# Kernel tuning notes

Hardware: AMD Instinct MI355X
Metric: run time of the kernel (lower is better)

Reference implementation:

```python
import jax, jax.numpy as jnp
import numpy as np

B, C, H, W = 64, 512, 8, 8
K = 100            # num_class
H1, HID, L = 64, 128, 32   # ae_hidden[0], fixed hidd, ae_latent
CLIP = 100.0       # CSSRClassifier.clip_len
RED = -0.1         # model='pcssr' -> -1, times gamma=0.1
PUSH_THRESH = 10000.0


def setup_inputs() -> dict:
    key = jax.random.key(0)
    ks = jax.random.split(key, 9)
    s = lambda fan_in: 1.0 / np.sqrt(fan_in)  # kaiming-ish 1x1 conv init scale
    return {
        "x": jax.random.normal(ks[0], (B, C, H, W), jnp.float32),
        "ycls": jax.random.randint(ks[1], (B,), 0, K),
        "safe_margin_all": jax.random.normal(ks[2], (K,), jnp.float32),
        "safe_distance_all": jax.random.normal(ks[3], (K,), jnp.float32),
        "W1": jax.random.normal(ks[4], (K, H1, C), jnp.float32) * s(C),
        "W2": jax.random.normal(ks[5], (K, HID, H1), jnp.float32) * s(H1),
        "W3": jax.random.normal(ks[6], (K, L, HID), jnp.float32) * s(HID),
        "prototypes": jax.random.normal(ks[7], (K, L, H, W), jnp.float32),
        "prototypes1": jax.random.normal(ks[8], (K, L, H, W), jnp.float32),
    }


def reference(x, ycls, safe_margin_all, safe_distance_all, W1, W2, W3, prototypes, prototypes1):
    P = H * W
    xf = x.reshape(B, C, P)
    # per-class 1x1-conv encoder (tanh after every conv), batched over classes k
    h = jnp.tanh(jnp.einsum('koc,bcp->kbop', W1, xf))      # [K,B,H1,P]
    h = jnp.tanh(jnp.einsum('koi,kbip->kbop', W2, h))      # [K,B,HID,P]
    lt = jnp.tanh(jnp.einsum('koi,kbip->kbop', W3, h))     # [K,B,L,P]
    p = prototypes.reshape(K, 1, L, P)
    p1 = prototypes1.reshape(K, 1, L, P)
    # squared-L2 distance over channel dim, scaled by reduction, clipped
    er = jnp.clip(jnp.sum((lt - p) ** 2, axis=2) * RED, -CLIP, CLIP)    # [K,B,P]
    er1 = jnp.clip(jnp.sum((lt - p1) ** 2, axis=2) * RED, -CLIP, CLIP)  # [K,B,P]
    # training losses (pull on er1, push on er), vectorized across classes
    f = jnp.sum(er, axis=2)    # [K,B] spatial-summed errors
    f1 = jnp.sum(er1, axis=2)  # [K,B]
    cls_ids = jnp.arange(K)[:, None]
    mask_eq = (ycls[None, :] == cls_ids).astype(f.dtype)   # [K,B]
    n_eq = jnp.sum(mask_eq, axis=1)
    pull = jnp.sum(jnp.where(n_eq > 0,
                             jnp.sum(f1 * mask_eq, axis=1) / jnp.maximum(n_eq, 1.0),
                             0.0))
    comb = (1.0 - mask_eq) * (f < PUSH_THRESH).astype(f.dtype)
    n_comb = jnp.sum(comb, axis=1)
    push = jnp.sum(jnp.where(n_comb > 0,
                             jnp.sum(f * comb, axis=1) / jnp.maximum(n_comb, 1.0),
                             0.0))
    # cat per-class [B,1,H,W] errors along dim 1 -> [B,K,H,W]
    logits = jnp.transpose(er, (1, 0, 2)).reshape(B, K, H, W)
    logits1 = jnp.transpose(er1, (1, 0, 2)).reshape(B, K, H, W)
    return logits, logits1, pull, push
```

## Files before the change

### kernel.cpp

```cpp
#include <hip/hip_runtime.h>

typedef short  s16x8  __attribute__((ext_vector_type(8)));
typedef float  f32x16 __attribute__((ext_vector_type(16)));
typedef unsigned short u16;
typedef unsigned long long u64b;

#define MFMA32(a,b,c) __builtin_amdgcn_mfma_f32_32x32x16_bf16((a),(b),(c),0,0,0)
#define KCLS 100

__device__ __forceinline__ u16 f2bf(float f) {
  return (u16)(__builtin_bit_cast(unsigned, f) >> 16);
}

__device__ __forceinline__ float tanh_fast(float x) {
  float e = __builtin_amdgcn_exp2f(x * 2.8853900817779268f);
  return 1.0f - 2.0f * __builtin_amdgcn_rcpf(e + 1.0f);
}

__device__ __forceinline__ void ld_lds16(const void* g, void* l) {
  __builtin_amdgcn_global_load_lds(
      (const __attribute__((address_space(1))) unsigned char*)g,
      (__attribute__((address_space(3))) unsigned char*)l, 16, 0, 0);
}

__global__ void prep(const float* __restrict__ x, const float* __restrict__ w1,
                     const float* __restrict__ w2, const float* __restrict__ w3,
                     u16* __restrict__ xF, u16* __restrict__ W1F,
                     u16* __restrict__ W2F, u16* __restrict__ W3F,
                     float* __restrict__ out2) {
  __shared__ float tile[64][65];
  const int bid = blockIdx.x, t = threadIdx.x;
  if (bid == 0 && t < 2) out2[t] = 0.f;
  if (bid < 512) {
    const int b = bid >> 3, ck = bid & 7;
    #pragma unroll
    for (int j = 0; j < 4; j++) {
      int e4 = j * 1024 + t * 4;
      int c = e4 >> 6, p0 = e4 & 63;
      float4 v = *(const float4*)(x + ((size_t)b * 512 + ck * 64 + c) * 64 + p0);
      tile[c][p0] = v.x; tile[c][p0 + 1] = v.y; tile[c][p0 + 2] = v.z; tile[c][p0 + 3] = v.w;
    }
    __syncthreads();
    #pragma unroll
    for (int i = 0; i < 2; i++) {
      int s = i * 256 + t;
      int ksl = s >> 7, ph = (s >> 6) & 1, lane = s & 63;
      int cb = ksl * 16 + (lane >> 5) * 8, pp = ph * 32 + (lane & 31);
      u16 o[8];
      #pragma unroll
      for (int jj = 0; jj < 8; jj++) o[jj] = f2bf(tile[cb + jj][pp]);
      *(uint4*)(xF + (((size_t)b * 64 + (ck * 4 + ksl) * 2 + ph) * 512) + lane * 8) = *(uint4*)o;
    }
  } else if (bid < 1312) {
    int base = (bid - 512) * 512;
    #pragma unroll
    for (int i = 0; i < 2; i++) {
      int s = base + i * 256 + t;
      int frag = s >> 6, lane = s & 63;
      int k = frag >> 6, fr = frag & 63;
      int m = (fr & 1) * 32 + (lane & 31);
      int c0 = (fr >> 1) * 16 + (lane >> 5) * 8;
      const float* src = w1 + ((size_t)k * 64 + m) * 512 + c0;
      float4 a = *(const float4*)src, b4 = *(const float4*)(src + 4);
      u16 o[8] = { f2bf(a.x), f2bf(a.y), f2bf(a.z), f2bf(a.w),
                   f2bf(b4.x), f2bf(b4.y), f2bf(b4.z), f2bf(b4.w) };
      *(uint4*)(W1F + ((size_t)frag * 512) + lane * 8) = *(uint4*)o;
    }
  } else if (bid < 1512) {
    int base = (bid - 1312) * 512;
    #pragma unroll
    for (int i = 0; i < 2; i++) {
      int s = base + i * 256 + t;
      int frag = s >> 6, lane = s & 63;
      int k = frag >> 4, fr = frag & 15;
      int m = (fr & 3) * 32 + (lane & 31);
      int c0 = (fr >> 2) * 16 + (lane >> 5) * 8;
      const float* src = w2 + ((size_t)k * 128 + m) * 64 + c0;
      float4 a = *(const float4*)src, b4 = *(const float4*)(src + 4);
      u16 o[8] = { f2bf(a.x), f2bf(a.y), f2bf(a.z), f2bf(a.w),
                   f2bf(b4.x), f2bf(b4.y), f2bf(b4.z), f2bf(b4.w) };
      *(uint4*)(W2F + ((size_t)frag * 512) + lane * 8) = *(uint4*)o;
    }
  } else {
    int base = (bid - 1512) * 512;
    #pragma unroll
    for (int i = 0; i < 2; i++) {
      int s = base + i * 256 + t;
      int frag = s >> 6, lane = s & 63;
      int k = frag >> 3, kb = frag & 7;
      int m = lane & 31;
      int c0 = kb * 16 + (lane >> 5) * 8;
      const float* src = w3 + ((size_t)k * 32 + m) * 128 + c0;
      float4 a = *(const float4*)src, b4 = *(const float4*)(src + 4);
      u16 o[8] = { f2bf(a.x), f2bf(a.y), f2bf(a.z), f2bf(a.w),
                   f2bf(b4.x), f2bf(b4.y), f2bf(b4.z), f2bf(b4.w) };
      *(uint4*)(W3F + ((size_t)frag * 512) + lane * 8) = *(uint4*)o;
    }
  }
}

__global__ __launch_bounds__(256, 4) void cssr_main(
    const u16* __restrict__ W1F, const u16* __restrict__ W2F, const u16* __restrict__ W3F,
    const u16* __restrict__ xF, const float* __restrict__ protos,
    const float* __restrict__ protos1, float* __restrict__ out,
    float* __restrict__ fw, float* __restrict__ f1w)
{
  __shared__ u16 pool[16384];
  __shared__ float red[8];
  u16 (*sB)[2][4][512] = (u16(*)[2][4][512])pool;
  u16 (*h1f)[4][512]   = (u16(*)[4][512])(pool + 8192);
  u16 (*h2f)[4][512]   = (u16(*)[4][512])pool;

  const int bid = blockIdx.x;
  const int k = bid >> 5, b0 = (bid & 31) * 2;
  const int tid = threadIdx.x, w = tid >> 6, lane = tid & 63;
  const int nhalf = lane >> 5, nn = lane & 31;
  const int mt = w >> 1, ntp = w & 1;

  #pragma unroll
  for (int i = 0; i < 2; i++) {
    int f = 2 * w + i, ksl = f >> 2, nt = f & 3;
    const u16* gp = xF + (((size_t)(b0 + (nt >> 1)) * 64 + ksl * 2 + (nt & 1)) * 512) + lane * 8;
    ld_lds16(gp, &sB[0][ksl][nt][0]);
  }
  __syncthreads();

  f32x16 acc1[2] = {};
  for (int ch = 0; ch < 16; ch++) {
    const int pb = ch & 1;
    if (ch < 15) {
      #pragma unroll
      for (int i = 0; i < 2; i++) {
        int f = 2 * w + i, ksl = f >> 2, nt = f & 3;
        int g = (ch + 1) * 2 + ksl;
        const u16* gp = xF + (((size_t)(b0 + (nt >> 1)) * 64 + g * 2 + (nt & 1)) * 512) + lane * 8;
        ld_lds16(gp, &sB[pb ^ 1][ksl][nt][0]);
      }
    }
    #pragma unroll
    for (int ksl = 0; ksl < 2; ksl++) {
      int g = ch * 2 + ksl;
      s16x8 A = *(const s16x8*)(W1F + (((size_t)k * 64 + g * 2 + mt) * 512) + lane * 8);
      #pragma unroll
      for (int ntl = 0; ntl < 2; ntl++) {
        s16x8 B = *(const s16x8*)&sB[pb][ksl][ntp * 2 + ntl][lane * 8];
        acc1[ntl] = MFMA32(A, B, acc1[ntl]);
      }
    }
    __syncthreads();
  }

  #pragma unroll
  for (int ntl = 0; ntl < 2; ntl++) {
    int nt = ntp * 2 + ntl;
    #pragma unroll
    for (int g = 0; g < 4; g++) {
      u16 hv[4];
      #pragma unroll
      for (int q = 0; q < 4; q++) hv[q] = f2bf(tanh_fast(acc1[ntl][g * 4 + q]));
      int kbg = mt * 2 + (g >> 1);
      int tl  = (g & 1) * 32 + nn;
      *(u64b*)&h1f[kbg][nt][tl * 8 + nhalf * 4] = *(u64b*)hv;
    }
  }
  __syncthreads();

  f32x16 acc2[2][2] = {};
  #pragma unroll
  for (int kb = 0; kb < 4; kb++) {
    s16x8 A0 = *(const s16x8*)(W2F + (((size_t)k * 16 + kb * 4 + (mt * 2 + 0)) * 512) + lane * 8);
    s16x8 A1 = *(const s16x8*)(W2F + (((size_t)k * 16 + kb * 4 + (mt * 2 + 1)) * 512) + lane * 8);
    #pragma unroll
    for (int ntl = 0; ntl < 2; ntl++) {
      s16x8 B = *(const s16x8*)&h1f[kb][ntp * 2 + ntl][lane * 8];
      acc2[0][ntl] = MFMA32(A0, B, acc2[0][ntl]);
      acc2[1][ntl] = MFMA32(A1, B, acc2[1][ntl]);
    }
  }
  __syncthreads();

  #pragma unroll
  for (int i = 0; i < 2; i++) {
    #pragma unroll
    for (int ntl = 0; ntl < 2; ntl++) {
      int nt = ntp * 2 + ntl;
      #pragma unroll
      for (int g = 0; g < 4; g++) {
        u16 hv[4];
        #pragma unroll
        for (int q = 0; q < 4; q++) hv[q] = f2bf(tanh_fast(acc2[i][ntl][g * 4 + q]));
        int kbg2 = (mt * 2 + i) * 2 + (g >> 1);
        int tl   = (g & 1) * 32 + nn;
        *(u64b*)&h2f[kbg2][nt][tl * 8 + nhalf * 4] = *(u64b*)hv;
      }
    }
  }
  __syncthreads();

  f32x16 acc3 = {};
  #pragma unroll
  for (int kb = 0; kb < 8; kb++) {
    s16x8 A = *(const s16x8*)(W3F + (((size_t)k * 8 + kb) * 512) + lane * 8);
    s16x8 B = *(const s16x8*)&h2f[kb][w][lane * 8];
    acc3 = MFMA32(A, B, acc3);
  }

  const int b = b0 + (w >> 1);
  const int p = (w & 1) * 32 + nn;
  const float* pr  = protos  + (size_t)k * 2048;
  const float* pr1 = protos1 + (size_t)k * 2048;
  float d2 = 0.f, d21 = 0.f;
  #pragma unroll
  for (int g = 0; g < 4; g++) {
    #pragma unroll
    for (int q = 0; q < 4; q++) {
      int m = q + 8 * g + 4 * nhalf;
      float lt = tanh_fast(acc3[g * 4 + q]);
      float d = lt - pr [m * 64 + p];  d2  += d * d;
      float e = lt - pr1[m * 64 + p];  d21 += e * e;
    }
  }
  d2 += __shfl_xor(d2, 32); d21 += __shfl_xor(d21, 32);
  float er  = fminf(fmaxf(d2  * -0.1f, -100.f), 100.f);
  float er1 = fminf(fmaxf(d21 * -0.1f, -100.f), 100.f);
  if (nhalf == 0) {
    out[(size_t)b * 6400 + k * 64 + p]          = er;
    out[409600 + (size_t)b * 6400 + k * 64 + p] = er1;
  }
  float s = er, s1 = er1;
  s += __shfl_xor(s, 1);  s1 += __shfl_xor(s1, 1);
  s += __shfl_xor(s, 2);  s1 += __shfl_xor(s1, 2);
  s += __shfl_xor(s, 4);  s1 += __shfl_xor(s1, 4);
  s += __shfl_xor(s, 8);  s1 += __shfl_xor(s1, 8);
  s += __shfl_xor(s, 16); s1 += __shfl_xor(s1, 16);
  if (lane == 0) { red[w] = s; red[4 + w] = s1; }
  __syncthreads();
  if (tid < 2)      fw [k * 64 + b0 + tid]       = red[tid * 2] + red[tid * 2 + 1];
  else if (tid < 4) f1w[k * 64 + b0 + (tid - 2)] = red[4 + (tid - 2) * 2] + red[5 + (tid - 2) * 2];
}

__global__ void finalize(const float* __restrict__ f, const float* __restrict__ f1,
                         const int* __restrict__ ycls, float* __restrict__ out2) {
  const int k = blockIdx.x, b = threadIdx.x;
  float fv = f[k * 64 + b], f1v = f1[k * 64 + b];
  bool eq = (ycls[b] == k);
  bool cb = (!eq) && (fv < 10000.f);
  float s1 = eq ? f1v : 0.f, ne = eq ? 1.f : 0.f;
  float s  = cb ? fv  : 0.f, nc = cb ? 1.f : 0.f;
  #pragma unroll
  for (int o = 1; o < 64; o <<= 1) {
    s1 += __shfl_xor(s1, o); ne += __shfl_xor(ne, o);
    s  += __shfl_xor(s,  o); nc += __shfl_xor(nc, o);
  }
  if (b == 0) {
    if (ne > 0.f) atomicAdd(&out2[0], s1 / ne);
    if (nc > 0.f) atomicAdd(&out2[1], s / nc);
  }
}

extern "C" void kernel_launch(void* const* d_in, const int* in_sizes, int n_in,
                              void* d_out, int out_size, void* d_ws, size_t ws_size,
                              hipStream_t stream) {
  const float* x     = (const float*)d_in[0];
  const int*   ycls  = (const int*)d_in[1];
  const float* W1    = (const float*)d_in[4];
  const float* W2    = (const float*)d_in[5];
  const float* W3    = (const float*)d_in[6];
  const float* prot  = (const float*)d_in[7];
  const float* prot1 = (const float*)d_in[8];
  float* out = (float*)d_out;

  char* ws = (char*)d_ws;
  u16*  xFb = (u16*)(ws);
  u16*  W1F = (u16*)(ws + 4194304);
  u16*  W2F = (u16*)(ws + 10747904);
  u16*  W3F = (u16*)(ws + 12386304);
  float* fw  = (float*)(ws + 13205504);
  float* f1w = (float*)(ws + 13231104);

  prep<<<1612, 256, 0, stream>>>(x, W1, W2, W3, xFb, W1F, W2F, W3F, out + 819200);
  cssr_main<<<KCLS * 32, 256, 0, stream>>>(W1F, W2F, W3F, xFb, prot, prot1, out, fw, f1w);
  finalize<<<KCLS, 64, 0, stream>>>(fw, f1w, ycls, out + 819200);
}
```

Baseline: 151.0 us.

## Make each wave own a full sample-half chain and fuse finalize via last-block reduction

Restructures the main kernel so each wave computes all three encoder layers for its own (batch, spatial-half) column. Layer 1 now reads x fragments straight from global memory instead of through a double-buffered shared-memory pipeline, and intermediates stay in a private per-wave LDS slice, so block-wide barriers between layers go away. The separate finalize launch is replaced by atomic accumulation of per-class sums plus a last-block-done counter, whose final block computes pull and push. The cost is that each wave recomputes full W1/W2 work per column, which raises weight-fragment global loads, and the per-class sums now depend on atomics and a grid-wide completion counter.

```diff
diff --git a/kernel.cpp b/kernel.cpp
--- a/kernel.cpp
+++ b/kernel.cpp
@@ -17,20 +17,18 @@
   return 1.0f - 2.0f * __builtin_amdgcn_rcpf(e + 1.0f);
 }
 
-__device__ __forceinline__ void ld_lds16(const void* g, void* l) {
-  __builtin_amdgcn_global_load_lds(
-      (const __attribute__((address_space(1))) unsigned char*)g,
-      (__attribute__((address_space(3))) unsigned char*)l, 16, 0, 0);
-}
-
 __global__ void prep(const float* __restrict__ x, const float* __restrict__ w1,
                      const float* __restrict__ w2, const float* __restrict__ w3,
                      u16* __restrict__ xF, u16* __restrict__ W1F,
                      u16* __restrict__ W2F, u16* __restrict__ W3F,
+                     float* __restrict__ fz, unsigned* __restrict__ done,
                      float* __restrict__ out2) {
   __shared__ float tile[64][65];
   const int bid = blockIdx.x, t = threadIdx.x;
-  if (bid == 0 && t < 2) out2[t] = 0.f;
+  if (bid == 0) {
+    if (t < 2) out2[t] = 0.f;
+    if (t == 2) *done = 0u;
+  }
   if (bid < 512) {
     const int b = bid >> 3, ck = bid & 7;
     #pragma unroll
@@ -81,7 +79,7 @@
                    f2bf(b4.x), f2bf(b4.y), f2bf(b4.z), f2bf(b4.w) };
       *(uint4*)(W2F + ((size_t)frag * 512) + lane * 8) = *(uint4*)o;
     }
-  } else {
+  } else if (bid < 1612) {
     int base = (bid - 1512) * 512;
     #pragma unroll
     for (int i = 0; i < 2; i++) {
@@ -96,117 +94,91 @@
                    f2bf(b4.x), f2bf(b4.y), f2bf(b4.z), f2bf(b4.w) };
       *(uint4*)(W3F + ((size_t)frag * 512) + lane * 8) = *(uint4*)o;
     }
+  } else {
+    int i4 = (bid - 1612) * 256 + t;
+    if (i4 < 3200) {
+      float4 z = {0.f, 0.f, 0.f, 0.f};
+      *(float4*)(fz + (size_t)i4 * 4) = z;
+    }
   }
 }
 
 __global__ __launch_bounds__(256, 4) void cssr_main(
     const u16* __restrict__ W1F, const u16* __restrict__ W2F, const u16* __restrict__ W3F,
     const u16* __restrict__ xF, const float* __restrict__ protos,
-    const float* __restrict__ protos1, float* __restrict__ out,
-    float* __restrict__ fw, float* __restrict__ f1w)
+    const float* __restrict__ protos1, const int* __restrict__ ycls,
+    float* __restrict__ out, float* __restrict__ fw, float* __restrict__ f1w,
+    unsigned* __restrict__ done, float* __restrict__ out2)
 {
   __shared__ u16 pool[16384];
-  __shared__ float red[8];
-  u16 (*sB)[2][4][512] = (u16(*)[2][4][512])pool;
-  u16 (*h1f)[4][512]   = (u16(*)[4][512])(pool + 8192);
-  u16 (*h2f)[4][512]   = (u16(*)[4][512])pool;
+  __shared__ int isLast;
 
   const int bid = blockIdx.x;
   const int k = bid >> 5, b0 = (bid & 31) * 2;
   const int tid = threadIdx.x, w = tid >> 6, lane = tid & 63;
   const int nhalf = lane >> 5, nn = lane & 31;
-  const int mt = w >> 1, ntp = w & 1;
-
-  #pragma unroll
-  for (int i = 0; i < 2; i++) {
-    int f = 2 * w + i, ksl = f >> 2, nt = f & 3;
-    const u16* gp = xF + (((size_t)(b0 + (nt >> 1)) * 64 + ksl * 2 + (nt & 1)) * 512) + lane * 8;
-    ld_lds16(gp, &sB[0][ksl][nt][0]);
-  }
-  __syncthreads();
+  const int b = b0 + (w >> 1), ph = w & 1;
+
+  u16* wls = pool + (w << 12);
 
   f32x16 acc1[2] = {};
-  for (int ch = 0; ch < 16; ch++) {
-    const int pb = ch & 1;
-    if (ch < 15) {
-      #pragma unroll
-      for (int i = 0; i < 2; i++) {
-        int f = 2 * w + i, ksl = f >> 2, nt = f & 3;
-        int g = (ch + 1) * 2 + ksl;
-        const u16* gp = xF + (((size_t)(b0 + (nt >> 1)) * 64 + g * 2 + (nt & 1)) * 512) + lane * 8;
-        ld_lds16(gp, &sB[pb ^ 1][ksl][nt][0]);
-      }
-    }
-    #pragma unroll
-    for (int ksl = 0; ksl < 2; ksl++) {
-      int g = ch * 2 + ksl;
-      s16x8 A = *(const s16x8*)(W1F + (((size_t)k * 64 + g * 2 + mt) * 512) + lane * 8);
-      #pragma unroll
-      for (int ntl = 0; ntl < 2; ntl++) {
-        s16x8 B = *(const s16x8*)&sB[pb][ksl][ntp * 2 + ntl][lane * 8];
-        acc1[ntl] = MFMA32(A, B, acc1[ntl]);
-      }
-    }
-    __syncthreads();
-  }
-
-  #pragma unroll
-  for (int ntl = 0; ntl < 2; ntl++) {
-    int nt = ntp * 2 + ntl;
+  const u16* xb = xF + (((size_t)b * 64 + ph) * 512) + lane * 8;
+  const u16* wA = W1F + ((size_t)k * 64 * 512) + lane * 8;
+  #pragma unroll 4
+  for (int g = 0; g < 32; g++) {
+    s16x8 B  = *(const s16x8*)(xb + g * 1024);
+    s16x8 A0 = *(const s16x8*)(wA + g * 1024);
+    s16x8 A1 = *(const s16x8*)(wA + g * 1024 + 512);
+    acc1[0] = MFMA32(A0, B, acc1[0]);
+    acc1[1] = MFMA32(A1, B, acc1[1]);
+  }
+
+  #pragma unroll
+  for (int mt = 0; mt < 2; mt++) {
     #pragma unroll
     for (int g = 0; g < 4; g++) {
       u16 hv[4];
       #pragma unroll
-      for (int q = 0; q < 4; q++) hv[q] = f2bf(tanh_fast(acc1[ntl][g * 4 + q]));
-      int kbg = mt * 2 + (g >> 1);
+      for (int q = 0; q < 4; q++) hv[q] = f2bf(tanh_fast(acc1[mt][g * 4 + q]));
+      int kb = mt * 2 + (g >> 1);
+      int tl = (g & 1) * 32 + nn;
+      *(u64b*)&wls[kb * 512 + tl * 8 + nhalf * 4] = *(u64b*)hv;
+    }
+  }
+
+  f32x16 acc2[4] = {};
+  #pragma unroll
+  for (int kb = 0; kb < 4; kb++) {
+    s16x8 B = *(const s16x8*)&wls[kb * 512 + lane * 8];
+    #pragma unroll
+    for (int m4 = 0; m4 < 4; m4++) {
+      s16x8 A = *(const s16x8*)(W2F + (((size_t)k * 16) + kb * 4 + m4) * 512 + lane * 8);
+      acc2[m4] = MFMA32(A, B, acc2[m4]);
+    }
+  }
+
+  #pragma unroll
+  for (int m4 = 0; m4 < 4; m4++) {
+    #pragma unroll
+    for (int g = 0; g < 4; g++) {
+      u16 hv[4];
+      #pragma unroll
+      for (int q = 0; q < 4; q++) hv[q] = f2bf(tanh_fast(acc2[m4][g * 4 + q]));
+      int kb2 = m4 * 2 + (g >> 1);
       int tl  = (g & 1) * 32 + nn;
-      *(u64b*)&h1f[kbg][nt][tl * 8 + nhalf * 4] = *(u64b*)hv;
-    }
-  }
-  __syncthreads();
-
-  f32x16 acc2[2][2] = {};
-  #pragma unroll
-  for (int kb = 0; kb < 4; kb++) {
-    s16x8 A0 = *(const s16x8*)(W2F + (((size_t)k * 16 + kb * 4 + (mt * 2 + 0)) * 512) + lane * 8);
-    s16x8 A1 = *(const s16x8*)(W2F + (((size_t)k * 16 + kb * 4 + (mt * 2 + 1)) * 512) + lane * 8);
-    #pragma unroll
-    for (int ntl = 0; ntl < 2; ntl++) {
-      s16x8 B = *(const s16x8*)&h1f[kb][ntp * 2 + ntl][lane * 8];
-      acc2[0][ntl] = MFMA32(A0, B, acc2[0][ntl]);
-      acc2[1][ntl] = MFMA32(A1, B, acc2[1][ntl]);
-    }
-  }
-  __syncthreads();
-
-  #pragma unroll
-  for (int i = 0; i < 2; i++) {
-    #pragma unroll
-    for (int ntl = 0; ntl < 2; ntl++) {
-      int nt = ntp * 2 + ntl;
-      #pragma unroll
-      for (int g = 0; g < 4; g++) {
-        u16 hv[4];
-        #pragma unroll
-        for (int q = 0; q < 4; q++) hv[q] = f2bf(tanh_fast(acc2[i][ntl][g * 4 + q]));
-        int kbg2 = (mt * 2 + i) * 2 + (g >> 1);
-        int tl   = (g & 1) * 32 + nn;
-        *(u64b*)&h2f[kbg2][nt][tl * 8 + nhalf * 4] = *(u64b*)hv;
-      }
-    }
-  }
-  __syncthreads();
+      *(u64b*)&wls[kb2 * 512 + tl * 8 + nhalf * 4] = *(u64b*)hv;
+    }
+  }
 
   f32x16 acc3 = {};
   #pragma unroll
   for (int kb = 0; kb < 8; kb++) {
-    s16x8 A = *(const s16x8*)(W3F + (((size_t)k * 8 + kb) * 512) + lane * 8);
-    s16x8 B = *(const s16x8*)&h2f[kb][w][lane * 8];
+    s16x8 A = *(const s16x8*)(W3F + (((size_t)k * 8) + kb) * 512 + lane * 8);
+    s16x8 B = *(const s16x8*)&wls[kb * 512 + lane * 8];
     acc3 = MFMA32(A, B, acc3);
   }
 
-  const int b = b0 + (w >> 1);
-  const int p = (w & 1) * 32 + nn;
+  const int p = ph * 32 + nn;
   const float* pr  = protos  + (size_t)k * 2048;
   const float* pr1 = protos1 + (size_t)k * 2048;
   float d2 = 0.f, d21 = 0.f;
@@ -233,28 +205,39 @@
   s += __shfl_xor(s, 4);  s1 += __shfl_xor(s1, 4);
   s += __shfl_xor(s, 8);  s1 += __shfl_xor(s1, 8);
   s += __shfl_xor(s, 16); s1 += __shfl_xor(s1, 16);
-  if (lane == 0) { red[w] = s; red[4 + w] = s1; }
+  if (lane == 0) {
+    atomicAdd(&fw [k * 64 + b], s);
+    atomicAdd(&f1w[k * 64 + b], s1);
+  }
+
+  __threadfence();
+  if (tid == 0) isLast = (atomicAdd(done, 1u) == (unsigned)(KCLS * 32 - 1));
   __syncthreads();
-  if (tid < 2)      fw [k * 64 + b0 + tid]       = red[tid * 2] + red[tid * 2 + 1];
-  else if (tid < 4) f1w[k * 64 + b0 + (tid - 2)] = red[4 + (tid - 2) * 2] + red[5 + (tid - 2) * 2];
-}
-
-__global__ void finalize(const float* __restrict__ f, const float* __restrict__ f1,
-                         const int* __restrict__ ycls, float* __restrict__ out2) {
-  const int k = blockIdx.x, b = threadIdx.x;
-  float fv = f[k * 64 + b], f1v = f1[k * 64 + b];
-  bool eq = (ycls[b] == k);
-  bool cb = (!eq) && (fv < 10000.f);
-  float s1 = eq ? f1v : 0.f, ne = eq ? 1.f : 0.f;
-  float s  = cb ? fv  : 0.f, nc = cb ? 1.f : 0.f;
-  #pragma unroll
-  for (int o = 1; o < 64; o <<= 1) {
-    s1 += __shfl_xor(s1, o); ne += __shfl_xor(ne, o);
-    s  += __shfl_xor(s,  o); nc += __shfl_xor(nc, o);
-  }
-  if (b == 0) {
-    if (ne > 0.f) atomicAdd(&out2[0], s1 / ne);
-    if (nc > 0.f) atomicAdd(&out2[1], s / nc);
+  if (isLast) {
+    __threadfence();
+    int yv = ycls[lane];
+    float pull = 0.f, push = 0.f;
+    for (int k2 = w; k2 < KCLS; k2 += 4) {
+      float fv  = __hip_atomic_load(&fw [k2 * 64 + lane], __ATOMIC_RELAXED, __HIP_MEMORY_SCOPE_AGENT);
+      float f1v = __hip_atomic_load(&f1w[k2 * 64 + lane], __ATOMIC_RELAXED, __HIP_MEMORY_SCOPE_AGENT);
+      bool eq = (yv == k2);
+      bool cb = (!eq) && (fv < 10000.f);
+      float s1 = eq ? f1v : 0.f, ne = eq ? 1.f : 0.f;
+      float sv = cb ? fv  : 0.f, nc = cb ? 1.f : 0.f;
+      #pragma unroll
+      for (int o = 1; o < 64; o <<= 1) {
+        s1 += __shfl_xor(s1, o); ne += __shfl_xor(ne, o);
+        sv += __shfl_xor(sv, o); nc += __shfl_xor(nc, o);
+      }
+      if (lane == 0) {
+        if (ne > 0.f) pull += s1 / ne;
+        if (nc > 0.f) push += sv / nc;
+      }
+    }
+    if (lane == 0) {
+      atomicAdd(&out2[0], pull);
+      atomicAdd(&out2[1], push);
+    }
   }
 }
 
@@ -277,8 +260,10 @@
   u16*  W3F = (u16*)(ws + 12386304);
   float* fw  = (float*)(ws + 13205504);
   float* f1w = (float*)(ws + 13231104);
-
-  prep<<<1612, 256, 0, stream>>>(x, W1, W2, W3, xFb, W1F, W2F, W3F, out + 819200);
-  cssr_main<<<KCLS * 32, 256, 0, stream>>>(W1F, W2F, W3F, xFb, prot, prot1, out, fw, f1w);
-  finalize<<<KCLS, 64, 0, stream>>>(fw, f1w, ycls, out + 819200);
-}
+  unsigned* done = (unsigned*)(ws + 13256704);
+
+  prep<<<1625, 256, 0, stream>>>(x, W1, W2, W3, xFb, W1F, W2F, W3F,
+                                 fw, done, out + 819200);
+  cssr_main<<<KCLS * 32, 256, 0, stream>>>(W1F, W2F, W3F, xFb, prot, prot1, ycls,
+                                           out, fw, f1w, done, out + 819200);
+}
```

Measured after the change: 424.2 us. +180.9%, slower.

## Remap blocks to two classes per batch item with larger x staging chunks

Applied to the files above, without the earlier changes.

Each block now processes one batch sample for two classes, sharing the staged x tile across both classes, with one wave pair per class. The x staging loop fetches 8 K-slices per iteration instead of 2, cutting barrier count. Per-block spatial sums are written with atomics into buffers that the prep kernel now zeroes. This trades W1 reuse across batches for x reuse across classes and adds atomic traffic.

```diff
diff --git a/kernel.cpp b/kernel.cpp
--- a/kernel.cpp
+++ b/kernel.cpp
@@ -27,7 +27,7 @@
                      const float* __restrict__ w2, const float* __restrict__ w3,
                      u16* __restrict__ xF, u16* __restrict__ W1F,
                      u16* __restrict__ W2F, u16* __restrict__ W3F,
-                     float* __restrict__ out2) {
+                     float* __restrict__ fz, float* __restrict__ out2) {
   __shared__ float tile[64][65];
   const int bid = blockIdx.x, t = threadIdx.x;
   if (bid == 0 && t < 2) out2[t] = 0.f;
@@ -81,7 +81,7 @@
                    f2bf(b4.x), f2bf(b4.y), f2bf(b4.z), f2bf(b4.w) };
       *(uint4*)(W2F + ((size_t)frag * 512) + lane * 8) = *(uint4*)o;
     }
-  } else {
+  } else if (bid < 1612) {
     int base = (bid - 1512) * 512;
     #pragma unroll
     for (int i = 0; i < 2; i++) {
@@ -96,6 +96,12 @@
                    f2bf(b4.x), f2bf(b4.y), f2bf(b4.z), f2bf(b4.w) };
       *(uint4*)(W3F + ((size_t)frag * 512) + lane * 8) = *(uint4*)o;
     }
+  } else {
+    int i4 = (bid - 1612) * 256 + t;
+    if (i4 < 3200) {
+      float4 z = {0.f, 0.f, 0.f, 0.f};
+      *(float4*)(fz + (size_t)i4 * 4) = z;
+    }
   }
 }
 
@@ -106,61 +112,56 @@
     float* __restrict__ fw, float* __restrict__ f1w)
 {
   __shared__ u16 pool[16384];
-  __shared__ float red[8];
-  u16 (*sB)[2][4][512] = (u16(*)[2][4][512])pool;
-  u16 (*h1f)[4][512]   = (u16(*)[4][512])(pool + 8192);
-  u16 (*h2f)[4][512]   = (u16(*)[4][512])pool;
 
   const int bid = blockIdx.x;
-  const int k = bid >> 5, b0 = (bid & 31) * 2;
+  const int kp = bid >> 6, b = bid & 63;
   const int tid = threadIdx.x, w = tid >> 6, lane = tid & 63;
   const int nhalf = lane >> 5, nn = lane & 31;
-  const int mt = w >> 1, ntp = w & 1;
-
-  #pragma unroll
-  for (int i = 0; i < 2; i++) {
-    int f = 2 * w + i, ksl = f >> 2, nt = f & 3;
-    const u16* gp = xF + (((size_t)(b0 + (nt >> 1)) * 64 + ksl * 2 + (nt & 1)) * 512) + lane * 8;
-    ld_lds16(gp, &sB[0][ksl][nt][0]);
+  const int kk = w >> 1, mt = w & 1;
+  const int k = kp * 2 + kk;
+
+  const u16* xb = xF + ((size_t)b * 64) * 512;
+
+  #pragma unroll
+  for (int i = 0; i < 4; i++) {
+    int f = w * 4 + i, gksl = f >> 1, ph = f & 1;
+    ld_lds16(xb + ((size_t)(gksl * 2 + ph)) * 512 + lane * 8, &pool[f * 512]);
   }
   __syncthreads();
 
   f32x16 acc1[2] = {};
-  for (int ch = 0; ch < 16; ch++) {
-    const int pb = ch & 1;
-    if (ch < 15) {
-      #pragma unroll
-      for (int i = 0; i < 2; i++) {
-        int f = 2 * w + i, ksl = f >> 2, nt = f & 3;
-        int g = (ch + 1) * 2 + ksl;
-        const u16* gp = xF + (((size_t)(b0 + (nt >> 1)) * 64 + g * 2 + (nt & 1)) * 512) + lane * 8;
-        ld_lds16(gp, &sB[pb ^ 1][ksl][nt][0]);
+  for (int ci = 0; ci < 4; ci++) {
+    const int pb = ci & 1;
+    if (ci < 3) {
+      #pragma unroll
+      for (int i = 0; i < 4; i++) {
+        int f = w * 4 + i, gksl = f >> 1, ph = f & 1;
+        ld_lds16(xb + ((size_t)(((ci + 1) * 8 + gksl) * 2 + ph)) * 512 + lane * 8,
+                 &pool[(pb ^ 1) * 8192 + f * 512]);
       }
     }
     #pragma unroll
-    for (int ksl = 0; ksl < 2; ksl++) {
-      int g = ch * 2 + ksl;
-      s16x8 A = *(const s16x8*)(W1F + (((size_t)k * 64 + g * 2 + mt) * 512) + lane * 8);
-      #pragma unroll
-      for (int ntl = 0; ntl < 2; ntl++) {
-        s16x8 B = *(const s16x8*)&sB[pb][ksl][ntp * 2 + ntl][lane * 8];
-        acc1[ntl] = MFMA32(A, B, acc1[ntl]);
+    for (int ksl = 0; ksl < 8; ksl++) {
+      s16x8 A = *(const s16x8*)(W1F + (((size_t)k * 64 + (ci * 8 + ksl) * 2 + mt) * 512) + lane * 8);
+      #pragma unroll
+      for (int nt = 0; nt < 2; nt++) {
+        s16x8 B = *(const s16x8*)&pool[pb * 8192 + (ksl * 2 + nt) * 512 + lane * 8];
+        acc1[nt] = MFMA32(A, B, acc1[nt]);
       }
     }
     __syncthreads();
   }
 
   #pragma unroll
-  for (int ntl = 0; ntl < 2; ntl++) {
-    int nt = ntp * 2 + ntl;
+  for (int nt = 0; nt < 2; nt++) {
     #pragma unroll
     for (int g = 0; g < 4; g++) {
       u16 hv[4];
       #pragma unroll
-      for (int q = 0; q < 4; q++) hv[q] = f2bf(tanh_fast(acc1[ntl][g * 4 + q]));
-      int kbg = mt * 2 + (g >> 1);
-      int tl  = (g & 1) * 32 + nn;
-      *(u64b*)&h1f[kbg][nt][tl * 8 + nhalf * 4] = *(u64b*)hv;
+      for (int q = 0; q < 4; q++) hv[q] = f2bf(tanh_fast(acc1[nt][g * 4 + q]));
+      int kb = mt * 2 + (g >> 1);
+      int tl = (g & 1) * 32 + nn;
+      *(u64b*)&pool[kk * 4096 + (kb * 2 + nt) * 512 + tl * 8 + nhalf * 4] = *(u64b*)hv;
     }
   }
   __syncthreads();
@@ -168,30 +169,29 @@
   f32x16 acc2[2][2] = {};
   #pragma unroll
   for (int kb = 0; kb < 4; kb++) {
-    s16x8 A0 = *(const s16x8*)(W2F + (((size_t)k * 16 + kb * 4 + (mt * 2 + 0)) * 512) + lane * 8);
-    s16x8 A1 = *(const s16x8*)(W2F + (((size_t)k * 16 + kb * 4 + (mt * 2 + 1)) * 512) + lane * 8);
-    #pragma unroll
-    for (int ntl = 0; ntl < 2; ntl++) {
-      s16x8 B = *(const s16x8*)&h1f[kb][ntp * 2 + ntl][lane * 8];
-      acc2[0][ntl] = MFMA32(A0, B, acc2[0][ntl]);
-      acc2[1][ntl] = MFMA32(A1, B, acc2[1][ntl]);
-    }
-  }
-  __syncthreads();
-
-  #pragma unroll
-  for (int i = 0; i < 2; i++) {
-    #pragma unroll
-    for (int ntl = 0; ntl < 2; ntl++) {
-      int nt = ntp * 2 + ntl;
+    s16x8 A0 = *(const s16x8*)(W2F + (((size_t)k * 16 + kb * 4 + mt * 2 + 0) * 512) + lane * 8);
+    s16x8 A1 = *(const s16x8*)(W2F + (((size_t)k * 16 + kb * 4 + mt * 2 + 1) * 512) + lane * 8);
+    #pragma unroll
+    for (int nh = 0; nh < 2; nh++) {
+      s16x8 B = *(const s16x8*)&pool[kk * 4096 + (kb * 2 + nh) * 512 + lane * 8];
+      acc2[0][nh] = MFMA32(A0, B, acc2[0][nh]);
+      acc2[1][nh] = MFMA32(A1, B, acc2[1][nh]);
+    }
+  }
+  __syncthreads();
+
+  #pragma unroll
+  for (int m4l = 0; m4l < 2; m4l++) {
+    #pragma unroll
+    for (int nh = 0; nh < 2; nh++) {
       #pragma unroll
       for (int g = 0; g < 4; g++) {
         u16 hv[4];
         #pragma unroll
-        for (int q = 0; q < 4; q++) hv[q] = f2bf(tanh_fast(acc2[i][ntl][g * 4 + q]));
-        int kbg2 = (mt * 2 + i) * 2 + (g >> 1);
-        int tl   = (g & 1) * 32 + nn;
-        *(u64b*)&h2f[kbg2][nt][tl * 8 + nhalf * 4] = *(u64b*)hv;
+        for (int q = 0; q < 4; q++) hv[q] = f2bf(tanh_fast(acc2[m4l][nh][g * 4 + q]));
+        int kb2 = mt * 4 + m4l * 2 + (g >> 1);
+        int tl  = (g & 1) * 32 + nn;
+        *(u64b*)&pool[kk * 8192 + (kb2 * 2 + nh) * 512 + tl * 8 + nhalf * 4] = *(u64b*)hv;
       }
     }
   }
@@ -201,12 +201,11 @@
   #pragma unroll
   for (int kb = 0; kb < 8; kb++) {
     s16x8 A = *(const s16x8*)(W3F + (((size_t)k * 8 + kb) * 512) + lane * 8);
-    s16x8 B = *(const s16x8*)&h2f[kb][w][lane * 8];
+    s16x8 B = *(const s16x8*)&pool[kk * 8192 + (kb * 2 + mt) * 512 + lane * 8];
     acc3 = MFMA32(A, B, acc3);
   }
 
-  const int b = b0 + (w >> 1);
-  const int p = (w & 1) * 32 + nn;
+  const int p = mt * 32 + nn;
   const float* pr  = protos  + (size_t)k * 2048;
   const float* pr1 = protos1 + (size_t)k * 2048;
   float d2 = 0.f, d21 = 0.f;
@@ -233,10 +232,10 @@
   s += __shfl_xor(s, 4);  s1 += __shfl_xor(s1, 4);
   s += __shfl_xor(s, 8);  s1 += __shfl_xor(s1, 8);
   s += __shfl_xor(s, 16); s1 += __shfl_xor(s1, 16);
-  if (lane == 0) { red[w] = s; red[4 + w] = s1; }
-  __syncthreads();
-  if (tid < 2)      fw [k * 64 + b0 + tid]       = red[tid * 2] + red[tid * 2 + 1];
-  else if (tid < 4) f1w[k * 64 + b0 + (tid - 2)] = red[4 + (tid - 2) * 2] + red[5 + (tid - 2) * 2];
+  if (lane == 0) {
+    atomicAdd(&fw [k * 64 + b], s);
+    atomicAdd(&f1w[k * 64 + b], s1);
+  }
 }
 
 __global__ void finalize(const float* __restrict__ f, const float* __restrict__ f1,
@@ -278,7 +277,9 @@
   float* fw  = (float*)(ws + 13205504);
   float* f1w = (float*)(ws + 13231104);
 
-  prep<<<1612, 256, 0, stream>>>(x, W1, W2, W3, xFb, W1F, W2F, W3F, out + 819200);
-  cssr_main<<<KCLS * 32, 256, 0, stream>>>(W1F, W2F, W3F, xFb, prot, prot1, out, fw, f1w);
+  prep<<<1625, 256, 0, stream>>>(x, W1, W2, W3, xFb, W1F, W2F, W3F,
+                                 fw, out + 819200);
+  cssr_main<<<50 * 64, 256, 0, stream>>>(W1F, W2F, W3F, xFb, prot, prot1,
+                                         out, fw, f1w);
   finalize<<<KCLS, 64, 0, stream>>>(fw, f1w, ycls, out + 819200);
 }
```

Result: faster. 143.3 us (-5.1%).
